# Kernel optimization log

Hardware: AMD Instinct MI355X
Metric: run time of the kernel (lower is better)

The kernel has to match this reference:

```python
import jax, jax.numpy as jnp
import numpy as np

N_NODES = 50000
BN_EPS = 1e-5


def _gin_layer(x, src, dst, W1, b1, gamma, beta, W2, b2):
    # GINConv (eps=0): h = MLP(x + sum_{j->i} x_j)
    agg = jax.ops.segment_sum(x[src], dst, num_segments=N_NODES)  # [N, F]
    h = (x + agg) @ W1 + b1                                       # [N, H]
    # BatchNorm1d over node dim (training-mode batch statistics, biased var)
    mean = jnp.mean(h, axis=0)
    var = jnp.mean((h - mean) ** 2, axis=0)
    h = (h - mean) * jax.lax.rsqrt(var + BN_EPS) * gamma + beta
    h = jax.nn.relu(h)
    h = jax.nn.relu(h @ W2 + b2)
    return h


def setup_inputs() -> dict:
    key = jax.random.key(0)
    ks = jax.random.split(key, 16)
    F_in, H = 9, 256
    E = 800000
    x = jax.random.normal(ks[0], (N_NODES, F_in), dtype=jnp.float32)
    edge_index = jax.random.randint(ks[1], (2, E), 0, N_NODES, dtype=jnp.int64)

    def lin(k, fi, fo):
        s = 1.0 / np.sqrt(fi)
        kw, kb = jax.random.split(k)
        W = jax.random.uniform(kw, (fi, fo), jnp.float32, -s, s)
        b = jax.random.uniform(kb, (fo,), jnp.float32, -s, s)
        return W, b

    inp = {"x": x, "edge_index": edge_index}
    dims = [(F_in, H), (H, H), (H, H)]
    for i, (fi, fo) in enumerate(dims, start=1):
        W1, b1 = lin(ks[2 * i], fi, fo)
        W2, b2 = lin(ks[2 * i + 1], fo, fo)
        inp[f"W1_{i}"] = W1; inp[f"b1_{i}"] = b1
        inp[f"g_{i}"] = jnp.ones((fo,), jnp.float32)
        inp[f"be_{i}"] = jnp.zeros((fo,), jnp.float32)
        inp[f"W2_{i}"] = W2; inp[f"b2_{i}"] = b2
    return inp


def reference(x, edge_index,
              W1_1, b1_1, g_1, be_1, W2_1, b2_1,
              W1_2, b1_2, g_2, be_2, W2_2, b2_2,
              W1_3, b1_3, g_3, be_3, W2_3, b2_3):
    src, dst = edge_index[0], edge_index[1]
    h = _gin_layer(x, src, dst, W1_1, b1_1, g_1, be_1, W2_1, b2_1)
    h = jax.nn.relu(h)
    h = _gin_layer(h, src, dst, W1_2, b1_2, g_2, be_2, W2_2, b2_2)
    h = jax.nn.relu(h)
    h = _gin_layer(h, src, dst, W1_3, b1_3, g_3, be_3, W2_3, b2_3)
    h = jax.nn.relu(h)
    return jnp.sum(h, axis=0)  # [256]
```

## Files before the change

kernel.cpp:

```cpp
#include <hip/hip_runtime.h>

#define NN 50000
#define NE 800000
#define HD 256
#define BN_EPS 1e-5f

typedef __attribute__((ext_vector_type(8))) short bf16x8;
typedef __attribute__((ext_vector_type(8))) unsigned short ushort8;
typedef __attribute__((ext_vector_type(4))) float f32x4;

__device__ __forceinline__ float bf2f(unsigned short u) {
  union { unsigned int i; float f; } c; c.i = ((unsigned int)u) << 16; return c.f;
}
__device__ __forceinline__ unsigned short f2bf(float x) {
  union { float f; unsigned int i; } c; c.f = x;
  unsigned int r = (c.i + 0x7fffu + ((c.i >> 16) & 1u)) >> 16;
  return (unsigned short)r;
}

__global__ __launch_bounds__(1024) void k_zero(int* __restrict__ cursor, float* __restrict__ s_sum,
                                               float* __restrict__ s_sq, float* __restrict__ out) {
  int i = blockIdx.x * 1024 + threadIdx.x;
  if (i < NN) cursor[i] = 0;
  if (i < HD) { s_sum[i] = 0.f; s_sq[i] = 0.f; out[i] = 0.f; }
}

__global__ __launch_bounds__(256) void k_count(const int* __restrict__ dst, int* __restrict__ cnt) {
  int e = blockIdx.x * 256 + threadIdx.x;
  if (e < NE) atomicAdd(&cnt[dst[e]], 1);
}

__global__ __launch_bounds__(1024) void k_scan_a(const int* __restrict__ cnt,
                                                 int* __restrict__ rp, int* __restrict__ bsum) {
  __shared__ int wsum[16];
  int i = blockIdx.x * 1024 + threadIdx.x;
  int v = (i < NN) ? cnt[i] : 0;
  int lane = threadIdx.x & 63, wid = threadIdx.x >> 6;
  int s = v;
  #pragma unroll
  for (int off = 1; off < 64; off <<= 1) {
    int tv = __shfl_up(s, off);
    if (lane >= off) s += tv;
  }
  if (lane == 63) wsum[wid] = s;
  __syncthreads();
  if (wid == 0) {
    int ws = (lane < 16) ? wsum[lane] : 0;
    #pragma unroll
    for (int off = 1; off < 16; off <<= 1) {
      int tv = __shfl_up(ws, off);
      if (lane >= off) ws += tv;
    }
    if (lane < 16) wsum[lane] = ws;
  }
  __syncthreads();
  int excl = s - v + (wid > 0 ? wsum[wid - 1] : 0);
  if (i < NN) rp[i] = excl;
  if (threadIdx.x == 1023) bsum[blockIdx.x] = excl + v;
}

__global__ __launch_bounds__(1024) void k_scan_b(const int* __restrict__ bsum,
                                                 int* __restrict__ rp, int* __restrict__ cursor) {
  __shared__ int off_s;
  if (threadIdx.x < 64) {
    int v = ((int)threadIdx.x < (int)blockIdx.x && threadIdx.x < 49) ? bsum[threadIdx.x] : 0;
    #pragma unroll
    for (int o = 32; o > 0; o >>= 1) v += __shfl_xor(v, o);
    if (threadIdx.x == 0) off_s = v;
  }
  __syncthreads();
  int i = blockIdx.x * 1024 + threadIdx.x;
  if (i < NN) {
    int r = rp[i] + off_s;
    rp[i] = r;
    cursor[i] = r;
  }
  if (blockIdx.x == 0 && threadIdx.x == 0) rp[NN] = NE;
}

__global__ __launch_bounds__(256) void k_fill(const int* __restrict__ src, const int* __restrict__ dst,
                                              int* __restrict__ cursor, int* __restrict__ col) {
  int e = blockIdx.x * 256 + threadIdx.x;
  if (e < NE) {
    int p = atomicAdd(&cursor[dst[e]], 1);
    col[p] = src[e];
  }
}

__global__ __launch_bounds__(256) void k_prepW5(const float* __restrict__ Wa, const float* __restrict__ Wb,
    const float* __restrict__ Wc, const float* __restrict__ Wd, const float* __restrict__ We,
    unsigned short* __restrict__ out) {
  const float* W = (blockIdx.y == 0) ? Wa : (blockIdx.y == 1) ? Wb : (blockIdx.y == 2) ? Wc
                   : (blockIdx.y == 3) ? Wd : We;
  unsigned short* O = out + (size_t)blockIdx.y * HD * HD;
  int k = blockIdx.x, n = threadIdx.x;
  int nt = n >> 4, ks = k >> 5, lane = ((k >> 3) & 3) * 16 + (n & 15), j = k & 7;
  O[(size_t)((nt * 8 + ks) * 64 + lane) * 8 + j] = f2bf(W[k * 256 + n]);
}

__global__ __launch_bounds__(256) void k_agg9(const float* __restrict__ x,
    const int* __restrict__ rp, const int* __restrict__ col, float* __restrict__ u) {
  int i = blockIdx.x * 256 + threadIdx.x;
  if (i >= NN) return;
  float a[9];
  #pragma unroll
  for (int k = 0; k < 9; ++k) a[k] = x[(size_t)i * 9 + k];
  int e1 = rp[i + 1];
  for (int e = rp[i]; e < e1; ++e) {
    int nb = col[e];
    #pragma unroll
    for (int k = 0; k < 9; ++k) a[k] += x[(size_t)nb * 9 + k];
  }
  #pragma unroll
  for (int k = 0; k < 9; ++k) u[(size_t)i * 16 + k] = a[k];
}

__global__ __launch_bounds__(256) void k_l1gemm(const float* __restrict__ u,
    const float* __restrict__ W1, const float* __restrict__ b1,
    unsigned short* __restrict__ h, float* __restrict__ s_sum, float* __restrict__ s_sq) {
  __shared__ float Ws[9][256];
  int t = threadIdx.x;
  #pragma unroll
  for (int k = 0; k < 9; ++k) Ws[k][t] = W1[k * 256 + t];
  float bj = b1[t];
  __syncthreads();
  int r0 = blockIdx.x * 128;
  int r1 = min(r0 + 128, NN);
  float sum = 0.f, sq = 0.f;
  for (int r = r0; r < r1; ++r) {
    float acc = bj;
    #pragma unroll
    for (int k = 0; k < 9; ++k) acc = fmaf(u[(size_t)r * 16 + k], Ws[k][t], acc);
    h[(size_t)r * 256 + t] = f2bf(acc);
    sum += acc; sq += acc * acc;
  }
  atomicAdd(&s_sum[t], sum);
  atomicAdd(&s_sq[t], sq);
}

__global__ void k_finalize(float* __restrict__ s_sum, float* __restrict__ s_sq,
                           const float* __restrict__ g, const float* __restrict__ be,
                           float* __restrict__ scale, float* __restrict__ shift) {
  int j = threadIdx.x;
  float m = s_sum[j] / (float)NN;
  float v = s_sq[j] / (float)NN - m * m;
  v = fmaxf(v, 0.f);
  float sc = rsqrtf(v + BN_EPS) * g[j];
  scale[j] = sc;
  shift[j] = be[j] - m * sc;
  s_sum[j] = 0.f;
  s_sq[j] = 0.f;
}

__global__ __launch_bounds__(256) void k_agg256(const unsigned short* __restrict__ f,
    const int* __restrict__ rp, const int* __restrict__ col, unsigned short* __restrict__ u,
    int base, int lim) {
  int half = threadIdx.x >> 5;
  int lane32 = threadIdx.x & 31;
  int node = base + blockIdx.x * 8 + threadIdx.y * 2 + half;
  if (node >= lim) return;
  float acc[8];
  ushort8 v = *(const ushort8*)(f + (size_t)node * HD + lane32 * 8);
  #pragma unroll
  for (int j = 0; j < 8; ++j) acc[j] = bf2f(v[j]);
  int e0 = rp[node], e1 = rp[node + 1];
  int e = e0;
  for (; e + 3 < e1; e += 4) {
    int nb0 = col[e], nb1 = col[e + 1], nb2 = col[e + 2], nb3 = col[e + 3];
    ushort8 w0 = *(const ushort8*)(f + (size_t)nb0 * HD + lane32 * 8);
    ushort8 w1 = *(const ushort8*)(f + (size_t)nb1 * HD + lane32 * 8);
    ushort8 w2 = *(const ushort8*)(f + (size_t)nb2 * HD + lane32 * 8);
    ushort8 w3 = *(const ushort8*)(f + (size_t)nb3 * HD + lane32 * 8);
    #pragma unroll
    for (int j = 0; j < 8; ++j)
      acc[j] += (bf2f(w0[j]) + bf2f(w1[j])) + (bf2f(w2[j]) + bf2f(w3[j]));
  }
  for (; e < e1; ++e) {
    int nb = col[e];
    ushort8 w = *(const ushort8*)(f + (size_t)nb * HD + lane32 * 8);
    #pragma unroll
    for (int j = 0; j < 8; ++j) acc[j] += bf2f(w[j]);
  }
  ushort8 o;
  #pragma unroll
  for (int j = 0; j < 8; ++j) o[j] = f2bf(acc[j]);
  *(ushort8*)(u + (size_t)node * HD + lane32 * 8) = o;
}

template<bool PRE_BN, bool STATS, bool RELU, bool OUTSUM, bool WRITE>
__global__ __launch_bounds__(256, 2) void k_mfma_gemm(
    const unsigned short* __restrict__ A, const unsigned short* __restrict__ Bp,
    const float* __restrict__ bias, const float* __restrict__ scale, const float* __restrict__ shift,
    unsigned short* __restrict__ C,
    float* __restrict__ s_sum, float* __restrict__ s_sq, float* __restrict__ out)
{
  __shared__ unsigned short As[4][64 * 64];
  __shared__ float scLds[256], shLds[256];
  const int t = threadIdx.x;
  const int w = t >> 6;
  const int lane = t & 63;
  const int brow = blockIdx.x * 64;
  const bf16x8* Bf = (const bf16x8*)Bp;

  if (PRE_BN) { scLds[t] = scale[t]; shLds[t] = shift[t]; }

  #pragma unroll
  for (int tt = 0; tt < 4; ++tt) {
    #pragma unroll
    for (int hh = 0; hh < 2; ++hh) {
      int r0 = w * 16 + hh * 8;
      int row = r0 + (lane >> 3);
      int gp = (lane & 7) ^ (row & 7);
      int grow = brow + row; if (grow >= NN) grow = NN - 1;
      const unsigned short* gptr = A + (size_t)grow * HD + tt * 64 + gp * 8;
      __builtin_amdgcn_global_load_lds(
          (const __attribute__((address_space(1))) void*)gptr,
          (__attribute__((address_space(3))) void*)&As[tt][r0 * 64], 16, 0, 0);
    }
  }

  bf16x8 bfr[3][4];
  #pragma unroll
  for (int p = 0; p < 3; ++p)
    #pragma unroll
    for (int ntl = 0; ntl < 4; ++ntl)
      bfr[p][ntl] = Bf[(size_t)((w * 4 + ntl) * 8 + p) * 64 + lane];

  f32x4 zero; zero.x = zero.y = zero.z = zero.w = 0.f;
  f32x4 acc[4][4];
  #pragma unroll
  for (int i = 0; i < 4; ++i)
    #pragma unroll
    for (int j = 0; j < 4; ++j) acc[i][j] = zero;

  #pragma unroll
  for (int step = 0; step < 8; ++step) {
    const int tt = step >> 1, s = step & 1;
    if (s == 0) __syncthreads();
    const int cur = step % 3;
    float scv[8], shv[8];
    if (PRE_BN) {
      int kb = tt * 64 + s * 32 + (lane >> 4) * 8;
      #pragma unroll
      for (int j = 0; j < 8; ++j) { scv[j] = scLds[kb + j]; shv[j] = shLds[kb + j]; }
    }
    bf16x8 afr[4];
    #pragma unroll
    for (int mt = 0; mt < 4; ++mt) {
      int row = mt * 16 + (lane & 15);
      int g = s * 4 + (lane >> 4);
      int gp = g ^ (row & 7);
      afr[mt] = *(const bf16x8*)&As[tt][row * 64 + gp * 8];
      if (PRE_BN) {
        bf16x8 a = afr[mt];
        bf16x8 o;
        #pragma unroll
        for (int j = 0; j < 8; ++j) {
          float v = bf2f((unsigned short)a[j]);
          v = fmaxf(fmaf(v, scv[j], shv[j]), 0.f);
          o[j] = (short)f2bf(v);
        }
        afr[mt] = o;
      }
    }
    #pragma unroll
    for (int mt = 0; mt < 4; ++mt)
      #pragma unroll
      for (int ntl = 0; ntl < 4; ++ntl)
        acc[mt][ntl] = __builtin_amdgcn_mfma_f32_16x16x32_bf16(
            afr[mt], bfr[cur][ntl], acc[mt][ntl], 0, 0, 0);
    if (step < 5) {
      #pragma unroll
      for (int ntl = 0; ntl < 4; ++ntl)
        bfr[cur][ntl] = Bf[(size_t)((w * 4 + ntl) * 8 + step + 3) * 64 + lane];
    }
  }

  const int cl = lane & 15;
  const int rq = (lane >> 4) * 4;
  #pragma unroll
  for (int ntl = 0; ntl < 4; ++ntl) {
    const int cgl = w * 64 + ntl * 16 + cl;
    const float bv = bias[cgl];
    float s = 0.f, q = 0.f;
    #pragma unroll
    for (int mt = 0; mt < 4; ++mt) {
      #pragma unroll
      for (int i = 0; i < 4; ++i) {
        float v = acc[mt][ntl][i] + bv;
        if (RELU) v = fmaxf(v, 0.f);
        int grow = brow + mt * 16 + rq + i;
        bool valid = grow < NN;
        if (WRITE && valid) C[(size_t)grow * HD + cgl] = f2bf(v);
        if ((STATS || OUTSUM) && valid) { s += v; if (STATS) q += v * v; }
      }
    }
    if (STATS || OUTSUM) {
      s += __shfl_xor(s, 16); s += __shfl_xor(s, 32);
      if (STATS) { q += __shfl_xor(q, 16); q += __shfl_xor(q, 32); }
      if (lane < 16) {
        if (STATS) { atomicAdd(&s_sum[cgl], s); atomicAdd(&s_sq[cgl], q); }
        if (OUTSUM) atomicAdd(&out[cgl], s);
      }
    }
  }
}

extern "C" void kernel_launch(void* const* d_in, const int* in_sizes, int n_in,
                              void* d_out, int out_size, void* d_ws, size_t ws_size,
                              hipStream_t stream) {
  (void)in_sizes; (void)n_in; (void)out_size; (void)ws_size;
  const float* x  = (const float*)d_in[0];
  const int*  ei  = (const int*)d_in[1];
  const int*  src = ei;
  const int*  dst = ei + NE;
  const float* W1[3] = {(const float*)d_in[2],  (const float*)d_in[8],  (const float*)d_in[14]};
  const float* b1[3] = {(const float*)d_in[3],  (const float*)d_in[9],  (const float*)d_in[15]};
  const float* g_[3] = {(const float*)d_in[4],  (const float*)d_in[10], (const float*)d_in[16]};
  const float* be[3] = {(const float*)d_in[5],  (const float*)d_in[11], (const float*)d_in[17]};
  const float* W2[3] = {(const float*)d_in[6],  (const float*)d_in[12], (const float*)d_in[18]};
  const float* b2[3] = {(const float*)d_in[7],  (const float*)d_in[13], (const float*)d_in[19]};

  char* ws = (char*)d_ws;
  size_t o = 0;
  auto alloc = [&](size_t bytes) -> void* {
    void* p = ws + o;
    o += (bytes + 255) & ~(size_t)255;
    return p;
  };
  int*   rp     = (int*)alloc((size_t)(NN + 1) * 4);
  int*   cursor = (int*)alloc((size_t)NN * 4);
  int*   col    = (int*)alloc((size_t)NE * 4);
  int*   bsum   = (int*)alloc(64 * 4);
  float* u9     = (float*)alloc((size_t)NN * 16 * 4);
  unsigned short* ubf = (unsigned short*)alloc((size_t)NN * HD * 2);
  unsigned short* hbf = (unsigned short*)alloc((size_t)NN * HD * 2);
  unsigned short* fbf = (unsigned short*)alloc((size_t)NN * HD * 2);
  unsigned short* Wp  = (unsigned short*)alloc((size_t)5 * HD * HD * 2);
  float* s_sum  = (float*)alloc(HD * 4);
  float* s_sq   = (float*)alloc(HD * 4);
  float* scale  = (float*)alloc(HD * 4);
  float* shift  = (float*)alloc(HD * 4);
  float* out    = (float*)d_out;

  const int SCB = (NN + 1023) / 1024;

  k_zero<<<SCB, 1024, 0, stream>>>(cursor, s_sum, s_sq, out);
  k_count<<<(NE + 255) / 256, 256, 0, stream>>>(dst, cursor);
  k_scan_a<<<SCB, 1024, 0, stream>>>(cursor, rp, bsum);
  k_scan_b<<<SCB, 1024, 0, stream>>>(bsum, rp, cursor);
  k_fill<<<(NE + 255) / 256, 256, 0, stream>>>(src, dst, cursor, col);
  k_prepW5<<<dim3(256, 5), 256, 0, stream>>>(W2[0], W1[1], W2[1], W1[2], W2[2], Wp);

  unsigned short* WpA[5];
  for (int i = 0; i < 5; ++i) WpA[i] = Wp + (size_t)i * HD * HD;

  const int gemmGrid = (NN + 63) / 64;
  const int HN = 25000;
  dim3 aGridH((HN + 7) / 8);
  dim3 aBlk(64, 4);

  auto agg = [&](const unsigned short* f, unsigned short* u) {
    k_agg256<<<aGridH, aBlk, 0, stream>>>(f, rp, col, u, 0, HN);
    k_agg256<<<aGridH, aBlk, 0, stream>>>(f, rp, col, u, HN, NN);
  };

  k_agg9<<<(NN + 255) / 256, 256, 0, stream>>>(x, rp, col, u9);
  k_l1gemm<<<(NN + 127) / 128, 256, 0, stream>>>(u9, W1[0], b1[0], hbf, s_sum, s_sq);
  k_finalize<<<1, HD, 0, stream>>>(s_sum, s_sq, g_[0], be[0], scale, shift);
  k_mfma_gemm<true, false, true, false, true><<<gemmGrid, 256, 0, stream>>>(
      hbf, WpA[0], b2[0], scale, shift, fbf, nullptr, nullptr, nullptr);

  agg(fbf, ubf);
  k_mfma_gemm<false, true, false, false, true><<<gemmGrid, 256, 0, stream>>>(
      ubf, WpA[1], b1[1], nullptr, nullptr, hbf, s_sum, s_sq, nullptr);
  k_finalize<<<1, HD, 0, stream>>>(s_sum, s_sq, g_[1], be[1], scale, shift);
  k_mfma_gemm<true, false, true, false, true><<<gemmGrid, 256, 0, stream>>>(
      hbf, WpA[2], b2[1], scale, shift, fbf, nullptr, nullptr, nullptr);

  agg(fbf, ubf);
  k_mfma_gemm<false, true, false, false, true><<<gemmGrid, 256, 0, stream>>>(
      ubf, WpA[3], b1[2], nullptr, nullptr, hbf, s_sum, s_sq, nullptr);
  k_finalize<<<1, HD, 0, stream>>>(s_sum, s_sq, g_[2], be[2], scale, shift);
  k_mfma_gemm<true, false, true, true, false><<<gemmGrid, 256, 0, stream>>>(
      hbf, WpA[4], b2[2], scale, shift, nullptr, nullptr, nullptr, out);
}
```

Baseline: 492.9 us.

## Run layer-1 GEMM on MFMA with K padded to 64 and split aggregation in three

The layer-1 9-wide aggregation now writes bf16 rows padded to 64 columns. The scalar FP32 layer-1 GEMM is replaced by the templated MFMA GEMM with a single 64-wide K tile, and a new weight-packing kernel supplies the zero-padded W1. The neighbour aggregation is also split into three launches instead of two, likely to improve cache locality of the gathered features. This trades extra padded bytes and bf16 rounding of the layer-1 input for tensor-core throughput in place of a serial per-row FMA loop.

```diff
diff --git a/kernel.cpp b/kernel.cpp
--- a/kernel.cpp
+++ b/kernel.cpp
@@ -98,8 +98,16 @@
   O[(size_t)((nt * 8 + ks) * 64 + lane) * 8 + j] = f2bf(W[k * 256 + n]);
 }
 
-__global__ __launch_bounds__(256) void k_agg9(const float* __restrict__ x,
-    const int* __restrict__ rp, const int* __restrict__ col, float* __restrict__ u) {
+__global__ __launch_bounds__(256) void k_prepW1(const float* __restrict__ W, unsigned short* __restrict__ out) {
+  int k = blockIdx.x;
+  int n = threadIdx.x;
+  float v = (k < 9) ? W[k * 256 + n] : 0.f;
+  int nt = n >> 4, ks = k >> 5, lane = ((k >> 3) & 3) * 16 + (n & 15), j = k & 7;
+  out[(size_t)((nt * 2 + ks) * 64 + lane) * 8 + j] = f2bf(v);
+}
+
+__global__ __launch_bounds__(256) void k_agg9b(const float* __restrict__ x,
+    const int* __restrict__ rp, const int* __restrict__ col, unsigned short* __restrict__ u) {
   int i = blockIdx.x * 256 + threadIdx.x;
   if (i >= NN) return;
   float a[9];
@@ -111,31 +119,19 @@
     #pragma unroll
     for (int k = 0; k < 9; ++k) a[k] += x[(size_t)nb * 9 + k];
   }
-  #pragma unroll
-  for (int k = 0; k < 9; ++k) u[(size_t)i * 16 + k] = a[k];
-}
-
-__global__ __launch_bounds__(256) void k_l1gemm(const float* __restrict__ u,
-    const float* __restrict__ W1, const float* __restrict__ b1,
-    unsigned short* __restrict__ h, float* __restrict__ s_sum, float* __restrict__ s_sq) {
-  __shared__ float Ws[9][256];
-  int t = threadIdx.x;
-  #pragma unroll
-  for (int k = 0; k < 9; ++k) Ws[k][t] = W1[k * 256 + t];
-  float bj = b1[t];
-  __syncthreads();
-  int r0 = blockIdx.x * 128;
-  int r1 = min(r0 + 128, NN);
-  float sum = 0.f, sq = 0.f;
-  for (int r = r0; r < r1; ++r) {
-    float acc = bj;
-    #pragma unroll
-    for (int k = 0; k < 9; ++k) acc = fmaf(u[(size_t)r * 16 + k], Ws[k][t], acc);
-    h[(size_t)r * 256 + t] = f2bf(acc);
-    sum += acc; sq += acc * acc;
-  }
-  atomicAdd(&s_sum[t], sum);
-  atomicAdd(&s_sq[t], sq);
+  ushort8 o0 = {0,0,0,0,0,0,0,0}, o1 = {0,0,0,0,0,0,0,0}, oz = {0,0,0,0,0,0,0,0};
+  #pragma unroll
+  for (int k = 0; k < 8; ++k) o0[k] = f2bf(a[k]);
+  o1[0] = f2bf(a[8]);
+  unsigned short* up = u + (size_t)i * 64;
+  *(ushort8*)(up +  0) = o0;
+  *(ushort8*)(up +  8) = o1;
+  *(ushort8*)(up + 16) = oz;
+  *(ushort8*)(up + 24) = oz;
+  *(ushort8*)(up + 32) = oz;
+  *(ushort8*)(up + 40) = oz;
+  *(ushort8*)(up + 48) = oz;
+  *(ushort8*)(up + 56) = oz;
 }
 
 __global__ void k_finalize(float* __restrict__ s_sum, float* __restrict__ s_sq,
@@ -187,32 +183,33 @@
   *(ushort8*)(u + (size_t)node * HD + lane32 * 8) = o;
 }
 
-template<bool PRE_BN, bool STATS, bool RELU, bool OUTSUM, bool WRITE>
+template<int KT, bool PRE_BN, bool STATS, bool RELU, bool OUTSUM, bool WRITE>
 __global__ __launch_bounds__(256, 2) void k_mfma_gemm(
     const unsigned short* __restrict__ A, const unsigned short* __restrict__ Bp,
     const float* __restrict__ bias, const float* __restrict__ scale, const float* __restrict__ shift,
     unsigned short* __restrict__ C,
     float* __restrict__ s_sum, float* __restrict__ s_sq, float* __restrict__ out)
 {
-  __shared__ unsigned short As[4][64 * 64];
+  __shared__ unsigned short As[KT][64 * 64];
   __shared__ float scLds[256], shLds[256];
   const int t = threadIdx.x;
   const int w = t >> 6;
   const int lane = t & 63;
   const int brow = blockIdx.x * 64;
+  const int KD = KT * 64;
   const bf16x8* Bf = (const bf16x8*)Bp;
 
   if (PRE_BN) { scLds[t] = scale[t]; shLds[t] = shift[t]; }
 
   #pragma unroll
-  for (int tt = 0; tt < 4; ++tt) {
+  for (int tt = 0; tt < KT; ++tt) {
     #pragma unroll
     for (int hh = 0; hh < 2; ++hh) {
       int r0 = w * 16 + hh * 8;
       int row = r0 + (lane >> 3);
       int gp = (lane & 7) ^ (row & 7);
       int grow = brow + row; if (grow >= NN) grow = NN - 1;
-      const unsigned short* gptr = A + (size_t)grow * HD + tt * 64 + gp * 8;
+      const unsigned short* gptr = A + (size_t)grow * KD + tt * 64 + gp * 8;
       __builtin_amdgcn_global_load_lds(
           (const __attribute__((address_space(1))) void*)gptr,
           (__attribute__((address_space(3))) void*)&As[tt][r0 * 64], 16, 0, 0);
@@ -221,10 +218,12 @@
 
   bf16x8 bfr[3][4];
   #pragma unroll
-  for (int p = 0; p < 3; ++p)
+  for (int p = 0; p < 3; ++p) {
+    const int pp = (p < 2 * KT) ? p : 0;
     #pragma unroll
     for (int ntl = 0; ntl < 4; ++ntl)
-      bfr[p][ntl] = Bf[(size_t)((w * 4 + ntl) * 8 + p) * 64 + lane];
+      bfr[p][ntl] = Bf[(size_t)((w * 4 + ntl) * (2 * KT) + pp) * 64 + lane];
+  }
 
   f32x4 zero; zero.x = zero.y = zero.z = zero.w = 0.f;
   f32x4 acc[4][4];
@@ -234,7 +233,7 @@
     for (int j = 0; j < 4; ++j) acc[i][j] = zero;
 
   #pragma unroll
-  for (int step = 0; step < 8; ++step) {
+  for (int step = 0; step < 2 * KT; ++step) {
     const int tt = step >> 1, s = step & 1;
     if (s == 0) __syncthreads();
     const int cur = step % 3;
@@ -269,10 +268,10 @@
       for (int ntl = 0; ntl < 4; ++ntl)
         acc[mt][ntl] = __builtin_amdgcn_mfma_f32_16x16x32_bf16(
             afr[mt], bfr[cur][ntl], acc[mt][ntl], 0, 0, 0);
-    if (step < 5) {
+    if (step < 2 * KT - 3) {
       #pragma unroll
       for (int ntl = 0; ntl < 4; ++ntl)
-        bfr[cur][ntl] = Bf[(size_t)((w * 4 + ntl) * 8 + step + 3) * 64 + lane];
+        bfr[cur][ntl] = Bf[(size_t)((w * 4 + ntl) * (2 * KT) + step + 3) * 64 + lane];
     }
   }
 
@@ -332,11 +331,12 @@
   int*   cursor = (int*)alloc((size_t)NN * 4);
   int*   col    = (int*)alloc((size_t)NE * 4);
   int*   bsum   = (int*)alloc(64 * 4);
-  float* u9     = (float*)alloc((size_t)NN * 16 * 4);
+  unsigned short* u64b = (unsigned short*)alloc((size_t)NN * 64 * 2);
   unsigned short* ubf = (unsigned short*)alloc((size_t)NN * HD * 2);
   unsigned short* hbf = (unsigned short*)alloc((size_t)NN * HD * 2);
   unsigned short* fbf = (unsigned short*)alloc((size_t)NN * HD * 2);
   unsigned short* Wp  = (unsigned short*)alloc((size_t)5 * HD * HD * 2);
+  unsigned short* Wp1 = (unsigned short*)alloc((size_t)64 * HD * 2);
   float* s_sum  = (float*)alloc(HD * 4);
   float* s_sq   = (float*)alloc(HD * 4);
   float* scale  = (float*)alloc(HD * 4);
@@ -351,37 +351,40 @@
   k_scan_b<<<SCB, 1024, 0, stream>>>(bsum, rp, cursor);
   k_fill<<<(NE + 255) / 256, 256, 0, stream>>>(src, dst, cursor, col);
   k_prepW5<<<dim3(256, 5), 256, 0, stream>>>(W2[0], W1[1], W2[1], W1[2], W2[2], Wp);
+  k_prepW1<<<64, 256, 0, stream>>>(W1[0], Wp1);
 
   unsigned short* WpA[5];
   for (int i = 0; i < 5; ++i) WpA[i] = Wp + (size_t)i * HD * HD;
 
   const int gemmGrid = (NN + 63) / 64;
-  const int HN = 25000;
-  dim3 aGridH((HN + 7) / 8);
+  const int TN = 16672;
+  dim3 aGridT((TN + 7) / 8);
   dim3 aBlk(64, 4);
 
   auto agg = [&](const unsigned short* f, unsigned short* u) {
-    k_agg256<<<aGridH, aBlk, 0, stream>>>(f, rp, col, u, 0, HN);
-    k_agg256<<<aGridH, aBlk, 0, stream>>>(f, rp, col, u, HN, NN);
+    k_agg256<<<aGridT, aBlk, 0, stream>>>(f, rp, col, u, 0, TN);
+    k_agg256<<<aGridT, aBlk, 0, stream>>>(f, rp, col, u, TN, 2 * TN);
+    k_agg256<<<aGridT, aBlk, 0, stream>>>(f, rp, col, u, 2 * TN, NN);
   };
 
-  k_agg9<<<(NN + 255) / 256, 256, 0, stream>>>(x, rp, col, u9);
-  k_l1gemm<<<(NN + 127) / 128, 256, 0, stream>>>(u9, W1[0], b1[0], hbf, s_sum, s_sq);
+  k_agg9b<<<(NN + 255) / 256, 256, 0, stream>>>(x, rp, col, u64b);
+  k_mfma_gemm<1, false, true, false, false, true><<<gemmGrid, 256, 0, stream>>>(
+      u64b, Wp1, b1[0], nullptr, nullptr, hbf, s_sum, s_sq, nullptr);
   k_finalize<<<1, HD, 0, stream>>>(s_sum, s_sq, g_[0], be[0], scale, shift);
-  k_mfma_gemm<true, false, true, false, true><<<gemmGrid, 256, 0, stream>>>(
+  k_mfma_gemm<4, true, false, true, false, true><<<gemmGrid, 256, 0, stream>>>(
       hbf, WpA[0], b2[0], scale, shift, fbf, nullptr, nullptr, nullptr);
 
   agg(fbf, ubf);
-  k_mfma_gemm<false, true, false, false, true><<<gemmGrid, 256, 0, stream>>>(
+  k_mfma_gemm<4, false, true, false, false, true><<<gemmGrid, 256, 0, stream>>>(
       ubf, WpA[1], b1[1], nullptr, nullptr, hbf, s_sum, s_sq, nullptr);
   k_finalize<<<1, HD, 0, stream>>>(s_sum, s_sq, g_[1], be[1], scale, shift);
-  k_mfma_gemm<true, false, true, false, true><<<gemmGrid, 256, 0, stream>>>(
+  k_mfma_gemm<4, true, false, true, false, true><<<gemmGrid, 256, 0, stream>>>(
       hbf, WpA[2], b2[1], scale, shift, fbf, nullptr, nullptr, nullptr);
 
   agg(fbf, ubf);
-  k_mfma_gemm<false, true, false, false, true><<<gemmGrid, 256, 0, stream>>>(
+  k_mfma_gemm<4, false, true, false, false, true><<<gemmGrid, 256, 0, stream>>>(
       ubf, WpA[3], b1[2], nullptr, nullptr, hbf, s_sum, s_sq, nullptr);
   k_finalize<<<1, HD, 0, stream>>>(s_sum, s_sq, g_[2], be[2], scale, shift);
-  k_mfma_gemm<true, false, true, true, false><<<gemmGrid, 256, 0, stream>>>(
+  k_mfma_gemm<4, true, false, true, true, false><<<gemmGrid, 256, 0, stream>>>(
       hbf, WpA[4], b2[2], scale, shift, nullptr, nullptr, nullptr, out);
 }
```

Measured after the change: 497.7 us. About the same (+1.0%).
